# Optimization experiments

Measured on AMD Instinct MI355X. Metric: run time of the kernel, lower is better.

The kernel has to match this reference:

```python
import jax, jax.numpy as jnp
import numpy as np

# ---- static config (from init_kwargs) ----
SCALE = 1.0
N = 16384
DX = SCALE / N          # grid step = cutoff / 2
CUTOFF = 2.0 * DX
SQRT2 = float(np.sqrt(2.0))


def circ_conv(x, w):
    """Circularly-padded 1D cross-correlation (torch Conv1d, padding_mode='circular').
    x: [B, Cin, N], w: [Cout, Cin, K] (K odd). Returns [B, Cout, N]."""
    p = w.shape[-1] // 2
    xp = jnp.concatenate([x[..., -p:], x, x[..., :p]], axis=-1)
    return jax.lax.conv_general_dilated(
        xp, w, window_strides=(1,), padding='VALID',
        dimension_numbers=('NCH', 'OIH', 'NCH'))


def setup_inputs() -> dict:
    key = jax.random.key(0)
    ks = jax.random.split(key, 8)
    x = jax.random.normal(ks[0], (1024, 1, N), dtype=jnp.float32)
    # centered 4th-order accurate first-derivative stencil (acc=4), scaled by 1/dx
    deriv = np.array([1.0 / 12.0, -2.0 / 3.0, 0.0, 2.0 / 3.0, -1.0 / 12.0],
                     dtype=np.float32) / DX
    deriv_w = jnp.asarray(deriv).reshape(1, 1, 5)
    # discrete Box filter of width cutoff = 2*dx (trapezoidal weights)
    filt_w = jnp.asarray(np.array([0.25, 0.5, 0.25], dtype=np.float32)).reshape(1, 1, 3)
    # BasicNet(in=2, mid=[6,3], out=1, k=5, bias=True): kaiming-ish scaled init
    def conv_init(k, cout, cin, ks_):
        return jax.random.normal(k, (cout, cin, ks_), dtype=jnp.float32) / np.sqrt(cin * ks_)
    W1 = conv_init(ks[1], 6, 2, 5); b1 = jax.random.normal(ks[2], (6,), dtype=jnp.float32) * 0.01
    W2 = conv_init(ks[3], 3, 6, 5); b2 = jax.random.normal(ks[4], (3,), dtype=jnp.float32) * 0.01
    W3 = conv_init(ks[5], 1, 3, 5); b3 = jax.random.normal(ks[6], (1,), dtype=jnp.float32) * 0.01
    return {"x": x, "deriv_w": deriv_w, "filt_w": filt_w,
            "W1": W1, "b1": b1, "W2": W2, "b2": b2, "W3": W3, "b3": b3}


def reference(x, deriv_w, filt_w, W1, b1, W2, b2, W3, b3):
    xdiff = circ_conv(x, deriv_w)                                # [B,1,N]
    feat = jnp.concatenate([xdiff, x - circ_conv(x, filt_w)], axis=1)  # [B,2,N]
    h = jax.nn.elu(circ_conv(feat, W1) + b1[None, :, None])      # [B,6,N]
    h = jax.nn.elu(circ_conv(h, W2) + b2[None, :, None])         # [B,3,N]
    cs = jax.nn.elu(circ_conv(h, W3) + b3[None, :, None])        # [B,1,N]
    cs = jnp.clip(cs, 0.0, 1.0)                                  # Hardtanh(bounds)
    y = (cs * CUTOFF) ** 2 * jnp.abs(xdiff) * xdiff
    return circ_conv(SQRT2 * y, deriv_w)
```

## Files before the change

kernel.cpp:

```cpp
#include <hip/hip_runtime.h>
#include <math.h>

#define NN 16384
#define T 500
#define TILES 33

typedef float f2 __attribute__((ext_vector_type(2)));

__device__ __forceinline__ f2 elu2(f2 v) {
    f2 e;
    e.x = __expf(v.x);
    e.y = __expf(v.y);
    const f2 zero = (f2)0.0f;
    return __builtin_elementwise_max(v, zero)
         + __builtin_elementwise_min(e - 1.0f, zero);
}

__global__ void smag_setup(const float* __restrict__ dw,
                           const float* __restrict__ fw,
                           const float* __restrict__ W1,
                           float* __restrict__ cw)
{
    const int t = threadIdx.x;
    if (t < 54) {
        const int c = t / 9;
        const int m = (t % 9) - 4;
        float acc = 0.0f;
        #pragma unroll
        for (int k = 0; k < 5; ++k) {
            int j = m + 4 - k;
            if (j >= 0 && j <= 4) acc += W1[c * 10 + k] * dw[j];
        }
        if (m >= -2 && m <= 2) acc += W1[c * 10 + 5 + (m + 2)];
        #pragma unroll
        for (int i = 0; i < 3; ++i) {
            int k = m + 3 - i;
            if (k >= 0 && k <= 4) acc -= fw[i] * W1[c * 10 + 5 + k];
        }
        cw[t] = acc;
    }
}

__global__ __launch_bounds__(256, 8)
void smag_t5(const float* __restrict__ x,
             const float* __restrict__ dw,
             const float* __restrict__ cw,
             const float* __restrict__ b1,
             const float* __restrict__ W2, const float* __restrict__ b2,
             const float* __restrict__ W3, const float* __restrict__ b3,
             float* __restrict__ out)
{
    const int blk = (int)(blockIdx.x % TILES);
    const int row = (int)(blockIdx.x / TILES);
    const int tb  = blk * T;
    const int tid = threadIdx.x;
    const float* __restrict__ xr = x   + (size_t)row * NN;
    float* __restrict__ outr     = out + (size_t)row * NN;

    __shared__ __align__(16) float sm[4608];
    float* const sh1 = sm;
    float* const sy  = sm;
    float* const sh2 = sm + 3072;

    const float d0 = dw[0], d1 = dw[1], d2 = dw[2], d3 = dw[3], d4 = dw[4];

    f2 xd_m;
    {
        const int p = 2 * tid - 6;
        f2 G[6];
        #pragma unroll
        for (int i = 0; i < 6; ++i) {
            int g = (tb + p - 4 + 2 * i + NN) & (NN - 1);
            G[i] = *(const f2*)(xr + g);
        }
        f2 w9[9] = {G[0], {G[0].y, G[1].x}, G[1], {G[1].y, G[2].x}, G[2],
                    {G[2].y, G[3].x}, G[3], {G[3].y, G[4].x}, G[4]};
        #pragma unroll
        for (int c = 0; c < 6; ++c) {
            f2 a = (f2)b1[c];
            #pragma unroll
            for (int m = 0; m < 9; ++m)
                a = a + w9[m] * cw[c * 9 + m];
            *(f2*)(sh1 + c * 512 + p + 6) = elu2(a);
        }
        f2 a12 = {G[3].y, G[4].x};
        f2 a34 = {G[4].y, G[5].x};
        xd_m = G[3] * d0 + a12 * d1 + G[4] * d2 + a34 * d3 + G[5] * d4;
    }
    __syncthreads();

    if (tid < 254) {
        const int q = 2 * tid - 4;
        f2 acc0 = (f2)b2[0], acc1 = (f2)b2[1], acc2 = (f2)b2[2];
        #pragma unroll
        for (int ci = 0; ci < 6; ++ci) {
            const float* hb = sh1 + ci * 512 + q + 4;
            f2 H0 = *(f2*)(hb);
            f2 H1 = *(f2*)(hb + 2);
            f2 H2 = *(f2*)(hb + 4);
            f2 ha[5] = {H0, {H0.y, H1.x}, H1, {H1.y, H2.x}, H2};
            #pragma unroll
            for (int k = 0; k < 5; ++k) {
                acc0 = acc0 + ha[k] * W2[0 * 30 + ci * 5 + k];
                acc1 = acc1 + ha[k] * W2[1 * 30 + ci * 5 + k];
                acc2 = acc2 + ha[k] * W2[2 * 30 + ci * 5 + k];
            }
        }
        *(f2*)(sh2 + 0 * 512 + q + 4) = elu2(acc0);
        *(f2*)(sh2 + 1 * 512 + q + 4) = elu2(acc1);
        *(f2*)(sh2 + 2 * 512 + q + 4) = elu2(acc2);
    }
    __syncthreads();

    const float B3v = b3[0];
    const float K = 1.41421356237309515f * (float)(2.0/16384.0) * (float)(2.0/16384.0);
    if (tid < 252) {
        const int q = 2 * tid - 2;
        f2 a = (f2)B3v;
        #pragma unroll
        for (int ci = 0; ci < 3; ++ci) {
            const float* hb = sh2 + ci * 512 + q + 2;
            f2 H0 = *(f2*)(hb);
            f2 H1 = *(f2*)(hb + 2);
            f2 H2 = *(f2*)(hb + 4);
            f2 ha1 = {H0.y, H1.x};
            f2 ha3 = {H1.y, H2.x};
            a = a + H0 * W3[ci * 5 + 0] + ha1 * W3[ci * 5 + 1] + H1 * W3[ci * 5 + 2]
                  + ha3 * W3[ci * 5 + 3] + H2 * W3[ci * 5 + 4];
        }
        f2 cs = __builtin_elementwise_min(__builtin_elementwise_max(a, (f2)0.0f), (f2)1.0f);
        f2 axd = __builtin_elementwise_abs(xd_m);
        f2 y = (cs * cs) * (axd * xd_m) * K;
        *(f2*)(sy + q + 2) = y;
    }
    __syncthreads();

    if (tid < 250) {
        const int s = 2 * tid;
        f2 Y0 = *(f2*)(sy + s);
        f2 Y1 = *(f2*)(sy + s + 2);
        f2 Y2 = *(f2*)(sy + s + 4);
        f2 a12 = {Y0.y, Y1.x};
        f2 a34 = {Y1.y, Y2.x};
        f2 o = Y0 * d0 + a12 * d1 + Y1 * d2 + a34 * d3 + Y2 * d4;
        *(f2*)(outr + ((tb + s) & (NN - 1))) = o;
    }
}

extern "C" void kernel_launch(void* const* d_in, const int* in_sizes, int n_in,
                              void* d_out, int out_size, void* d_ws, size_t ws_size,
                              hipStream_t stream) {
    const float* x  = (const float*)d_in[0];
    const float* dw = (const float*)d_in[1];
    const float* fw = (const float*)d_in[2];
    const float* W1 = (const float*)d_in[3];
    const float* b1 = (const float*)d_in[4];
    const float* W2 = (const float*)d_in[5];
    const float* b2 = (const float*)d_in[6];
    const float* W3 = (const float*)d_in[7];
    const float* b3 = (const float*)d_in[8];
    float* out = (float*)d_out;
    float* cw  = (float*)d_ws;

    hipLaunchKernelGGL(smag_setup, dim3(1), dim3(64), 0, stream, dw, fw, W1, cw);

    const int B = 1024;
    dim3 grid(B * TILES);
    dim3 block(256);
    hipLaunchKernelGGL(smag_t5, grid, block, 0, stream,
                       x, dw, cw, b1, W2, b2, W3, b3, out);
}
```

Before: 97.20 us.

## Pack two batch rows per thread and stage input tile in shared memory

Each block now handles two batch rows at once. Every thread works on one spatial position and keeps the pair of rows in a float2, replacing the old scheme of two adjacent positions of a single row. The input tile is first staged into LDS, and all layers use an inline-asm v_pk_fma_f32 with a broadcast scalar weight. Tile size drops to 236 with 70 tiles per row pair. This removes the cross-lane shuffles needed to build shifted float2 windows and gives packed FMAs with no permutes, at the cost of an extra LDS staging pass, scalar (non-vectorized) global loads and stores, and larger halo overhead relative to the tile size.

```diff
diff --git a/kernel.cpp b/kernel.cpp
--- a/kernel.cpp
+++ b/kernel.cpp
@@ -2,18 +2,21 @@
 #include <math.h>
 
 #define NN 16384
-#define T 500
-#define TILES 33
+#define T 236
+#define TILES 70
 
 typedef float f2 __attribute__((ext_vector_type(2)));
 
+__device__ __forceinline__ void pkfma(f2& acc, f2 x, float w) {
+    f2 ws = {w, w};
+    asm("v_pk_fma_f32 %0, %1, %2, %0" : "+v"(acc) : "v"(x), "s"(ws));
+}
+
 __device__ __forceinline__ f2 elu2(f2 v) {
-    f2 e;
-    e.x = __expf(v.x);
-    e.y = __expf(v.y);
-    const f2 zero = (f2)0.0f;
-    return __builtin_elementwise_max(v, zero)
-         + __builtin_elementwise_min(e - 1.0f, zero);
+    f2 r;
+    r.x = fmaxf(v.x, 0.0f) + fminf(__expf(v.x) - 1.0f, 0.0f);
+    r.y = fmaxf(v.y, 0.0f) + fminf(__expf(v.y) - 1.0f, 0.0f);
+    return r;
 }
 
 __global__ void smag_setup(const float* __restrict__ dw,
@@ -42,7 +45,7 @@
 }
 
 __global__ __launch_bounds__(256, 8)
-void smag_t5(const float* __restrict__ x,
+void smag_bp(const float* __restrict__ x,
              const float* __restrict__ dw,
              const float* __restrict__ cw,
              const float* __restrict__ b1,
@@ -50,100 +53,112 @@
              const float* __restrict__ W3, const float* __restrict__ b3,
              float* __restrict__ out)
 {
-    const int blk = (int)(blockIdx.x % TILES);
-    const int row = (int)(blockIdx.x / TILES);
-    const int tb  = blk * T;
-    const int tid = threadIdx.x;
-    const float* __restrict__ xr = x   + (size_t)row * NN;
-    float* __restrict__ outr     = out + (size_t)row * NN;
+    const int tile = (int)(blockIdx.x % TILES);
+    const int rp   = (int)(blockIdx.x / TILES);
+    const int tb   = tile * T;
+    const int tid  = threadIdx.x;
+    const float* __restrict__ x0 = x + (size_t)(2 * rp) * NN;
+    const float* __restrict__ x1 = x0 + NN;
+    float* __restrict__ o0 = out + (size_t)(2 * rp) * NN;
+    float* __restrict__ o1 = o0 + NN;
 
-    __shared__ __align__(16) float sm[4608];
-    float* const sh1 = sm;
-    float* const sy  = sm;
-    float* const sh2 = sm + 3072;
+    __shared__ __align__(16) float sm[4952];
+    float* const sxi = sm;
+    float* const sh1 = sm + 512;
+    float* const sh2 = sm + 3488;
+    float* const sy  = sm + 512;
 
-    const float d0 = dw[0], d1 = dw[1], d2 = dw[2], d3 = dw[3], d4 = dw[4];
-
-    f2 xd_m;
     {
-        const int p = 2 * tid - 6;
-        f2 G[6];
-        #pragma unroll
-        for (int i = 0; i < 6; ++i) {
-            int g = (tb + p - 4 + 2 * i + NN) & (NN - 1);
-            G[i] = *(const f2*)(xr + g);
-        }
-        f2 w9[9] = {G[0], {G[0].y, G[1].x}, G[1], {G[1].y, G[2].x}, G[2],
-                    {G[2].y, G[3].x}, G[3], {G[3].y, G[4].x}, G[4]};
-        #pragma unroll
-        for (int c = 0; c < 6; ++c) {
-            f2 a = (f2)b1[c];
-            #pragma unroll
-            for (int m = 0; m < 9; ++m)
-                a = a + w9[m] * cw[c * 9 + m];
-            *(f2*)(sh1 + c * 512 + p + 6) = elu2(a);
-        }
-        f2 a12 = {G[3].y, G[4].x};
-        f2 a34 = {G[4].y, G[5].x};
-        xd_m = G[3] * d0 + a12 * d1 + G[4] * d2 + a34 * d3 + G[5] * d4;
+        const int pos = tid - 10;
+        const int g = (tb + pos + NN) & (NN - 1);
+        f2 v = {x0[g], x1[g]};
+        *(f2*)(sxi + 2 * tid) = v;
     }
     __syncthreads();
 
-    if (tid < 254) {
-        const int q = 2 * tid - 4;
-        f2 acc0 = (f2)b2[0], acc1 = (f2)b2[1], acc2 = (f2)b2[2];
+    if (tid < T + 12) {
+        const int q = tid - 6;
+        const float* xb = sxi + (q + 6) * 2;
+        f2 X[9];
+        #pragma unroll
+        for (int m = 0; m < 9; ++m) X[m] = *(const f2*)(xb + 2 * m);
+        #pragma unroll
+        for (int c = 0; c < 6; ++c) {
+            f2 a = {b1[c], b1[c]};
+            #pragma unroll
+            for (int m = 0; m < 9; ++m) pkfma(a, X[m], cw[c * 9 + m]);
+            *(f2*)(sh1 + c * 496 + (q + 6) * 2) = elu2(a);
+        }
+    }
+    __syncthreads();
+
+    if (tid < T + 8) {
+        const int u = tid - 4;
+        f2 a0 = {b2[0], b2[0]};
+        f2 a1 = {b2[1], b2[1]};
+        f2 a2 = {b2[2], b2[2]};
         #pragma unroll
         for (int ci = 0; ci < 6; ++ci) {
-            const float* hb = sh1 + ci * 512 + q + 4;
-            f2 H0 = *(f2*)(hb);
-            f2 H1 = *(f2*)(hb + 2);
-            f2 H2 = *(f2*)(hb + 4);
-            f2 ha[5] = {H0, {H0.y, H1.x}, H1, {H1.y, H2.x}, H2};
+            const float* hb = sh1 + ci * 496 + (u + 4) * 2;
+            f2 H[5];
+            #pragma unroll
+            for (int k = 0; k < 5; ++k) H[k] = *(const f2*)(hb + 2 * k);
             #pragma unroll
             for (int k = 0; k < 5; ++k) {
-                acc0 = acc0 + ha[k] * W2[0 * 30 + ci * 5 + k];
-                acc1 = acc1 + ha[k] * W2[1 * 30 + ci * 5 + k];
-                acc2 = acc2 + ha[k] * W2[2 * 30 + ci * 5 + k];
+                pkfma(a0, H[k], W2[0 * 30 + ci * 5 + k]);
+                pkfma(a1, H[k], W2[1 * 30 + ci * 5 + k]);
+                pkfma(a2, H[k], W2[2 * 30 + ci * 5 + k]);
             }
         }
-        *(f2*)(sh2 + 0 * 512 + q + 4) = elu2(acc0);
-        *(f2*)(sh2 + 1 * 512 + q + 4) = elu2(acc1);
-        *(f2*)(sh2 + 2 * 512 + q + 4) = elu2(acc2);
+        *(f2*)(sh2 + 0 * 488 + (u + 4) * 2) = elu2(a0);
+        *(f2*)(sh2 + 1 * 488 + (u + 4) * 2) = elu2(a1);
+        *(f2*)(sh2 + 2 * 488 + (u + 4) * 2) = elu2(a2);
     }
     __syncthreads();
 
     const float B3v = b3[0];
+    const float d0 = dw[0], d1 = dw[1], d2 = dw[2], d3 = dw[3], d4 = dw[4];
     const float K = 1.41421356237309515f * (float)(2.0/16384.0) * (float)(2.0/16384.0);
-    if (tid < 252) {
-        const int q = 2 * tid - 2;
-        f2 a = (f2)B3v;
+    if (tid < T + 4) {
+        const int v = tid - 2;
+        f2 a = {B3v, B3v};
         #pragma unroll
         for (int ci = 0; ci < 3; ++ci) {
-            const float* hb = sh2 + ci * 512 + q + 2;
-            f2 H0 = *(f2*)(hb);
-            f2 H1 = *(f2*)(hb + 2);
-            f2 H2 = *(f2*)(hb + 4);
-            f2 ha1 = {H0.y, H1.x};
-            f2 ha3 = {H1.y, H2.x};
-            a = a + H0 * W3[ci * 5 + 0] + ha1 * W3[ci * 5 + 1] + H1 * W3[ci * 5 + 2]
-                  + ha3 * W3[ci * 5 + 3] + H2 * W3[ci * 5 + 4];
+            const float* hb = sh2 + ci * 488 + (v + 2) * 2;
+            #pragma unroll
+            for (int k = 0; k < 5; ++k)
+                pkfma(a, *(const f2*)(hb + 2 * k), W3[ci * 5 + k]);
         }
-        f2 cs = __builtin_elementwise_min(__builtin_elementwise_max(a, (f2)0.0f), (f2)1.0f);
-        f2 axd = __builtin_elementwise_abs(xd_m);
-        f2 y = (cs * cs) * (axd * xd_m) * K;
-        *(f2*)(sy + q + 2) = y;
+        f2 xd = {0.0f, 0.0f};
+        const float* xb = sxi + (v + 8) * 2;
+        pkfma(xd, *(const f2*)(xb + 0), d0);
+        pkfma(xd, *(const f2*)(xb + 2), d1);
+        pkfma(xd, *(const f2*)(xb + 4), d2);
+        pkfma(xd, *(const f2*)(xb + 6), d3);
+        pkfma(xd, *(const f2*)(xb + 8), d4);
+        f2 y;
+        {
+            float c0 = fminf(fmaxf(a.x, 0.0f), 1.0f);
+            float c1 = fminf(fmaxf(a.y, 0.0f), 1.0f);
+            y.x = (c0 * c0 * K) * fabsf(xd.x) * xd.x;
+            y.y = (c1 * c1 * K) * fabsf(xd.y) * xd.y;
+        }
+        *(f2*)(sy + (v + 2) * 2) = y;
     }
     __syncthreads();
 
-    if (tid < 250) {
-        const int s = 2 * tid;
-        f2 Y0 = *(f2*)(sy + s);
-        f2 Y1 = *(f2*)(sy + s + 2);
-        f2 Y2 = *(f2*)(sy + s + 4);
-        f2 a12 = {Y0.y, Y1.x};
-        f2 a34 = {Y1.y, Y2.x};
-        f2 o = Y0 * d0 + a12 * d1 + Y1 * d2 + a34 * d3 + Y2 * d4;
-        *(f2*)(outr + ((tb + s) & (NN - 1))) = o;
+    if (tid < T) {
+        const int s = tid;
+        f2 o = {0.0f, 0.0f};
+        const float* yb = sy + s * 2;
+        pkfma(o, *(const f2*)(yb + 0), d0);
+        pkfma(o, *(const f2*)(yb + 2), d1);
+        pkfma(o, *(const f2*)(yb + 4), d2);
+        pkfma(o, *(const f2*)(yb + 6), d3);
+        pkfma(o, *(const f2*)(yb + 8), d4);
+        const int g = (tb + s) & (NN - 1);
+        o0[g] = o.x;
+        o1[g] = o.y;
     }
 }
 
@@ -165,8 +180,8 @@
     hipLaunchKernelGGL(smag_setup, dim3(1), dim3(64), 0, stream, dw, fw, W1, cw);
 
     const int B = 1024;
-    dim3 grid(B * TILES);
+    dim3 grid((B / 2) * TILES);
     dim3 block(256);
-    hipLaunchKernelGGL(smag_t5, grid, block, 0, stream,
+    hipLaunchKernelGGL(smag_bp, grid, block, 0, stream,
                        x, dw, cw, b1, W2, b2, W3, b3, out);
 }
```

After: 113.3 us. 16.5% more time.
